# Optimization experiments

Hardware: AMD Instinct MI355X
Metric: run time of the kernel (lower is better)

## Reference

```python
import jax, jax.numpy as jnp
import numpy as np

B, N, C = 8, 4096, 640
H_HEADS = 5
HD = C // H_HEADS  # 128
KS = 5
FOCUS = 3.0
EPS = 1e-6


def setup_inputs() -> dict:
    key = jax.random.key(0)
    ks = jax.random.split(key, 12)
    s = 0.02
    return {
        "x1": jax.random.normal(ks[0], (B, N, C), jnp.float32),
        "x2": jax.random.normal(ks[1], (B, N, C), jnp.float32),
        "Wq": jax.random.normal(ks[2], (C, C), jnp.float32) * s,
        "Wkv": jax.random.normal(ks[3], (2 * C, C), jnp.float32) * s,
        "Wproj": jax.random.normal(ks[4], (C, C), jnp.float32) * s,
        "bproj": jax.random.normal(ks[5], (C,), jnp.float32) * s,
        "dwc_w": jax.random.normal(ks[6], (HD, 1, KS, KS), jnp.float32) * s,
        "dwc_b": jax.random.normal(ks[7], (HD,), jnp.float32) * s,
        "scale": jax.random.normal(ks[8], (1, 1, C), jnp.float32) * s,
        "pos_enc": jax.random.normal(ks[9], (1, N, C), jnp.float32) * s,
        "H": 64,
        "W": 64,
    }


def _split_heads(t):
    # [B, N, C] -> [(B*h), N, hd]
    b, n, c = t.shape
    return t.reshape(b, n, H_HEADS, HD).transpose(0, 2, 1, 3).reshape(b * H_HEADS, n, HD)


def reference(x1, x2, Wq, Wkv, Wproj, bproj, dwc_w, dwc_b, scale, pos_enc, H, W):
    b, n, c = x1.shape
    # note the module's naming swap: self.q projects x2 into v
    v = x2 @ Wq.T                               # [B,N,C]
    kv = (x1 @ Wkv.T).reshape(b, n, 2, c)       # sr_ratio == 1 path
    k = kv[:, :, 0, :] + pos_enc
    q = kv[:, :, 1, :]

    sc = jax.nn.softplus(scale)                 # [1,1,C]
    q = (jax.nn.relu(q) + EPS) / sc
    k = (jax.nn.relu(k) + EPS) / sc
    q_norm = jnp.linalg.norm(q, axis=-1, keepdims=True)
    k_norm = jnp.linalg.norm(k, axis=-1, keepdims=True)
    q = q ** FOCUS
    k = k ** FOCUS
    q = q / jnp.linalg.norm(q, axis=-1, keepdims=True) * q_norm
    k = k / jnp.linalg.norm(k, axis=-1, keepdims=True) * k_norm

    q, k, v = _split_heads(q), _split_heads(k), _split_heads(v)  # [(B*h), N, hd]
    i, j, cc, d = q.shape[-2], k.shape[-2], k.shape[-1], v.shape[-1]
    z = 1.0 / (jnp.einsum('bic,bc->bi', q, k.sum(axis=1)) + EPS)  # [(B*h), N]
    if i * j * (cc + d) > cc * d * (i + j):
        kv2 = jnp.einsum('bjc,bjd->bcd', k, v)                    # [(B*h), hd, hd]
        x = jnp.einsum('bic,bcd,bi->bid', q, kv2, z)
    else:
        qk = jnp.einsum('bic,bjc->bij', q, k)
        x = jnp.einsum('bij,bjd,bi->bid', qk, v, z)

    # depthwise conv feature map on v: 'b (w h) c -> b c w h'
    num = int(round(n ** 0.5))
    fm = v.reshape(v.shape[0], num, num, HD).transpose(0, 3, 1, 2)  # [(B*h), hd, num, num]
    fm = jax.lax.conv_general_dilated(
        fm, dwc_w, window_strides=(1, 1), padding=((KS // 2, KS // 2),) * 2,
        dimension_numbers=('NCHW', 'OIHW', 'NCHW'), feature_group_count=HD)
    fm = fm + dwc_b[None, :, None, None]
    fm = fm.transpose(0, 2, 3, 1).reshape(v.shape[0], n, HD)

    x = x + fm
    # '(b h) n c -> b n (h c)'
    x = x.reshape(b, H_HEADS, n, HD).transpose(0, 2, 1, 3).reshape(b, n, c)
    return x @ Wproj.T + bproj
```

## Files before the change

kernel.cpp:

```cpp
#include <hip/hip_runtime.h>
#include <math.h>

constexpr int CB  = 8;
constexpr int CN  = 4096;
constexpr int CC  = 640;
constexpr int CNH = 5;
constexpr int CHD = 128;
constexpr int CM  = CB * CN;
constexpr float CEPS = 1e-6f;
constexpr int NCH = 8;

typedef __attribute__((ext_vector_type(8))) short bf16x8;
typedef __attribute__((ext_vector_type(4))) float f32x4;

typedef __attribute__((address_space(1))) const unsigned int gas_u32;
typedef __attribute__((address_space(3))) unsigned int las_u32;

__device__ __forceinline__ void gload16(const void* g, void* l) {
    __builtin_amdgcn_global_load_lds((gas_u32*)g, (las_u32*)l, 16, 0, 0);
}

__device__ __forceinline__ short f2bf(float x) {
    unsigned u = __float_as_uint(x);
    unsigned r = (u + 0x7fffu + ((u >> 16) & 1u)) >> 16;
    return (short)r;
}
__device__ __forceinline__ float b2f(unsigned short u) {
    return __uint_as_float(((unsigned)u) << 16);
}

__global__ void softplus_k(const float* __restrict__ scale, float* __restrict__ sc) {
    int t = threadIdx.x;
    if (t < CC) sc[t] = log1pf(expf(scale[t]));
}

__global__ __launch_bounds__(256) void cvt_bf16(const float* __restrict__ src,
                                                unsigned short* __restrict__ dst, int n8) {
    int i = blockIdx.x * 256 + threadIdx.x;
    const int stride = gridDim.x * 256;
    for (; i < n8; i += stride) {
        float4 f0 = *(const float4*)(src + (size_t)i * 8);
        float4 f1 = *(const float4*)(src + (size_t)i * 8 + 4);
        bf16x8 h;
        h[0]=f2bf(f0.x); h[1]=f2bf(f0.y); h[2]=f2bf(f0.z); h[3]=f2bf(f0.w);
        h[4]=f2bf(f1.x); h[5]=f2bf(f1.y); h[6]=f2bf(f1.z); h[7]=f2bf(f1.w);
        *(bf16x8*)(dst + (size_t)i * 8) = h;
    }
}

template<bool BIAS, bool OUTBF>
__global__ __launch_bounds__(256) void gemm_bf16b(const unsigned short* __restrict__ Abf,
                                                  const unsigned short* __restrict__ Bbf,
                                                  void* __restrict__ Co,
                                                  const float* __restrict__ bias,
                                                  int Kr, int Nr) {
    __shared__ unsigned short lA[4096];
    __shared__ unsigned short lB[4096];
    const int t  = threadIdx.x;
    const int m0 = blockIdx.y * 128;
    const int n0 = blockIdx.x * 128;
    const int l  = t & 63, w = t >> 6, wr = w >> 1, wc = w & 1;

    const int cp0 = w * 64 + l;
    const int cp1 = cp0 + 256;
    const int s0 = cp0 ^ (((cp0 >> 2) & 7) ^ ((cp0 >> 4) & 1));
    const int s1 = cp1 ^ (((cp1 >> 2) & 7) ^ ((cp1 >> 4) & 1));
    const size_t gA0 = (size_t)(m0 + (s0 >> 2)) * Kr + (s0 & 3) * 8;
    const size_t gA1 = (size_t)(m0 + (s1 >> 2)) * Kr + (s1 & 3) * 8;
    const size_t gB0 = (size_t)(n0 + (s0 >> 2)) * Kr + (s0 & 3) * 8;
    const size_t gB1 = (size_t)(n0 + (s1 >> 2)) * Kr + (s1 & 3) * 8;
    unsigned short* lA0 = lA + w * 512;
    unsigned short* lA1 = lA + 2048 + w * 512;
    unsigned short* lB0 = lB + w * 512;
    unsigned short* lB1 = lB + 2048 + w * 512;

    const int offA = ((wr * 64 + (l & 15)) * 64 + (l >> 4) * 16) ^ ((l & 7) << 4);
    const int offB = ((wc * 64 + (l & 15)) * 64 + (l >> 4) * 16) ^ ((l & 7) << 4);

    f32x4 acc[4][4];
    #pragma unroll
    for (int i = 0; i < 4; ++i)
        #pragma unroll
        for (int j = 0; j < 4; ++j) acc[i][j] = (f32x4){0.f, 0.f, 0.f, 0.f};

    for (int k0 = 0; k0 < Kr; k0 += 32) {
        gload16(Abf + gA0 + k0, lA0);
        gload16(Abf + gA1 + k0, lA1);
        gload16(Bbf + gB0 + k0, lB0);
        gload16(Bbf + gB1 + k0, lB1);
        __syncthreads();
        bf16x8 af[4], bfv[4];
        #pragma unroll
        for (int i = 0; i < 4; ++i) {
            af[i]  = *(const bf16x8*)((const char*)lA + offA + i * 1024);
            bfv[i] = *(const bf16x8*)((const char*)lB + offB + i * 1024);
        }
        #pragma unroll
        for (int i = 0; i < 4; ++i)
            #pragma unroll
            for (int j = 0; j < 4; ++j)
                acc[i][j] = __builtin_amdgcn_mfma_f32_16x16x32_bf16(af[i], bfv[j], acc[i][j], 0, 0, 0);
        __syncthreads();
    }

    #pragma unroll
    for (int j = 0; j < 4; ++j) {
        const int n = n0 + wc * 64 + j * 16 + (l & 15);
        const float bv = BIAS ? bias[n] : 0.f;
        #pragma unroll
        for (int i = 0; i < 4; ++i) {
            const int m = m0 + wr * 64 + i * 16 + (l >> 4) * 4;
            #pragma unroll
            for (int r = 0; r < 4; ++r) {
                float val = acc[i][j][r] + bv;
                if (OUTBF) ((unsigned short*)Co)[(size_t)(m + r) * Nr + n] = (unsigned short)f2bf(val);
                else       ((float*)Co)[(size_t)(m + r) * Nr + n] = val;
            }
        }
    }
}

__global__ __launch_bounds__(256) void rowtrans2(const unsigned short* __restrict__ qg,
                                                 const unsigned short* __restrict__ kg,
                                                 const float* __restrict__ pos,
                                                 const float* __restrict__ sc,
                                                 unsigned short* __restrict__ qt,
                                                 unsigned short* __restrict__ kt) {
    const int m = blockIdx.x;
    const int n = m & (CN - 1);
    const int t = threadIdx.x;
    float qv[3], kv[3];
    float s2q = 0.f, s6q = 0.f, s2k = 0.f, s6k = 0.f;
    #pragma unroll
    for (int i = 0; i < 3; ++i) {
        int c = t + i * 256;
        if (c < CC) {
            float scv = sc[c];
            float qq = b2f(qg[(size_t)m * CC + c]);
            qq = (fmaxf(qq, 0.f) + CEPS) / scv;
            float kk = b2f(kg[(size_t)m * CC + c]) + pos[(size_t)n * CC + c];
            kk = (fmaxf(kk, 0.f) + CEPS) / scv;
            qv[i] = qq; kv[i] = kk;
            float q2 = qq * qq, k2 = kk * kk;
            s2q += q2; s6q += q2 * q2 * q2;
            s2k += k2; s6k += k2 * k2 * k2;
        } else { qv[i] = 0.f; kv[i] = 0.f; }
    }
    #pragma unroll
    for (int o = 32; o > 0; o >>= 1) {
        s2q += __shfl_down(s2q, o);
        s6q += __shfl_down(s6q, o);
        s2k += __shfl_down(s2k, o);
        s6k += __shfl_down(s6k, o);
    }
    __shared__ float red[4][4];
    const int lane = t & 63, w = t >> 6;
    if (lane == 0) { red[0][w] = s2q; red[1][w] = s6q; red[2][w] = s2k; red[3][w] = s6k; }
    __syncthreads();
    float t2q = red[0][0] + red[0][1] + red[0][2] + red[0][3];
    float t6q = red[1][0] + red[1][1] + red[1][2] + red[1][3];
    float t2k = red[2][0] + red[2][1] + red[2][2] + red[2][3];
    float t6k = red[3][0] + red[3][1] + red[3][2] + red[3][3];
    const float qmul = sqrtf(t2q) / sqrtf(t6q);
    const float kmul = sqrtf(t2k) / sqrtf(t6k);
    #pragma unroll
    for (int i = 0; i < 3; ++i) {
        int c = t + i * 256;
        if (c < CC) {
            qt[(size_t)m * CC + c] = (unsigned short)f2bf(qv[i] * qv[i] * qv[i] * qmul);
            kt[(size_t)m * CC + c] = (unsigned short)f2bf(kv[i] * kv[i] * kv[i] * kmul);
        }
    }
}

__global__ __launch_bounds__(256) void kv2_partial(const unsigned short* __restrict__ kt,
                                                   const unsigned short* __restrict__ vb,
                                                   float* __restrict__ kv2p,
                                                   float* __restrict__ ksmp) {
    const int nc = blockIdx.x, bh = blockIdx.y;
    const int b = bh / CNH, h = bh % CNH;
    __shared__ float ks[32][132];
    __shared__ float vs[32][132];
    const int t = threadIdx.x;
    const int tx = t & 15, ty = t >> 4;
    float acc[8][8];
    #pragma unroll
    for (int i = 0; i < 8; ++i)
        #pragma unroll
        for (int j = 0; j < 8; ++j) acc[i][j] = 0.f;
    float ksacc = 0.f;
    const size_t mbase = (size_t)b * CN + (size_t)nc * 512;
    for (int tile = 0; tile < 16; ++tile) {
        const int nt0 = tile * 32;
        __syncthreads();
        #pragma unroll
        for (int r = 0; r < 2; ++r) {
            int idx = t + 256 * r;
            int nn = idx >> 4, c8 = (idx & 15) * 8;
            size_t g = (mbase + nt0 + nn) * CC + h * CHD + c8;
            bf16x8 hk = *(const bf16x8*)(kt + g);
            bf16x8 hv = *(const bf16x8*)(vb + g);
            float4 k0, k1, v0, v1;
            k0.x=b2f(hk[0]); k0.y=b2f(hk[1]); k0.z=b2f(hk[2]); k0.w=b2f(hk[3]);
            k1.x=b2f(hk[4]); k1.y=b2f(hk[5]); k1.z=b2f(hk[6]); k1.w=b2f(hk[7]);
            v0.x=b2f(hv[0]); v0.y=b2f(hv[1]); v0.z=b2f(hv[2]); v0.w=b2f(hv[3]);
            v1.x=b2f(hv[4]); v1.y=b2f(hv[5]); v1.z=b2f(hv[6]); v1.w=b2f(hv[7]);
            *(float4*)&ks[nn][c8]     = k0;
            *(float4*)&ks[nn][c8 + 4] = k1;
            *(float4*)&vs[nn][c8]     = v0;
            *(float4*)&vs[nn][c8 + 4] = v1;
        }
        __syncthreads();
        #pragma unroll 2
        for (int nn = 0; nn < 32; ++nn) {
            float4 a0 = *(const float4*)&ks[nn][ty*8];
            float4 a1 = *(const float4*)&ks[nn][ty*8+4];
            float4 b0 = *(const float4*)&vs[nn][tx*8];
            float4 b1 = *(const float4*)&vs[nn][tx*8+4];
            float a[8] = {a0.x,a0.y,a0.z,a0.w,a1.x,a1.y,a1.z,a1.w};
            float b[8] = {b0.x,b0.y,b0.z,b0.w,b1.x,b1.y,b1.z,b1.w};
            #pragma unroll
            for (int i = 0; i < 8; ++i)
                #pragma unroll
                for (int j = 0; j < 8; ++j)
                    acc[i][j] = fmaf(a[i], b[j], acc[i][j]);
        }
        if (t < 128) {
            #pragma unroll
            for (int nn = 0; nn < 32; ++nn) ksacc += ks[nn][t];
        }
    }
    float* outp = kv2p + ((size_t)bh * NCH + nc) * 16384;
    #pragma unroll
    for (int i = 0; i < 8; ++i) {
        float4 o0, o1;
        o0.x=acc[i][0]; o0.y=acc[i][1]; o0.z=acc[i][2]; o0.w=acc[i][3];
        o1.x=acc[i][4]; o1.y=acc[i][5]; o1.z=acc[i][6]; o1.w=acc[i][7];
        *(float4*)&outp[(ty*8+i)*128 + tx*8]     = o0;
        *(float4*)&outp[(ty*8+i)*128 + tx*8 + 4] = o1;
    }
    if (t < 128) ksmp[((size_t)bh * NCH + nc) * 128 + t] = ksacc;
}

__global__ __launch_bounds__(256) void kv2_reduce(const float* __restrict__ kv2p,
                                                  const float* __restrict__ ksmp,
                                                  unsigned short* __restrict__ kv2bf,
                                                  float* __restrict__ ksm) {
    const int bh = blockIdx.x, t = threadIdx.x;
    for (int o = t; o < 16384; o += 256) {
        const int d = o >> 7, c = o & 127;
        float s = 0.f;
        #pragma unroll
        for (int nc = 0; nc < NCH; ++nc)
            s += kv2p[((size_t)bh * NCH + nc) * 16384 + c * 128 + d];
        kv2bf[(size_t)bh * 16384 + o] = (unsigned short)f2bf(s);
    }
    if (t < 128) {
        float s = 0.f;
        #pragma unroll
        for (int nc = 0; nc < NCH; ++nc) s += ksmp[((size_t)bh * NCH + nc) * 128 + t];
        ksm[(size_t)bh * 128 + t] = s;
    }
}

__global__ __launch_bounds__(256) void attn_mfma(const unsigned short* __restrict__ qt,
                                                 const unsigned short* __restrict__ kv2bf,
                                                 const float* __restrict__ ksm,
                                                 unsigned short* __restrict__ attb) {
    const int nb = blockIdx.x, bh = blockIdx.y;
    const int b = bh / CNH, h = bh % CNH;
    __shared__ short lQ[16384];
    __shared__ short lKV[16384];
    __shared__ float zs[128];
    const int t = threadIdx.x;
    const int l = t & 63, w = t >> 6, wr = w >> 1, wc = w & 1;
    const size_t m0 = (size_t)b * CN + (size_t)nb * 128;

    const int srow0 = t >> 4;
    const int c16   = t & 15;
    float kreg[8];
    {
        const float* kp = ksm + (size_t)bh * 128 + c16 * 8;
        float4 k0 = *(const float4*)kp, k1 = *(const float4*)(kp + 4);
        kreg[0]=k0.x; kreg[1]=k0.y; kreg[2]=k0.z; kreg[3]=k0.w;
        kreg[4]=k1.x; kreg[5]=k1.y; kreg[6]=k1.z; kreg[7]=k1.w;
    }
    #pragma unroll
    for (int p = 0; p < 8; ++p) {
        const int row = srow0 + p * 16;
        const int st = (row * 256 + c16 * 16) ^ ((row & 7) << 4);
        bf16x8 hq = *(const bf16x8*)(qt + (m0 + row) * CC + h * CHD + c16 * 8);
        *(bf16x8*)((char*)lQ + st) = hq;
        float zp = 0.f;
        #pragma unroll
        for (int j = 0; j < 8; ++j) zp = fmaf(b2f((unsigned short)hq[j]), kreg[j], zp);
        zp += __shfl_xor(zp, 1);
        zp += __shfl_xor(zp, 2);
        zp += __shfl_xor(zp, 4);
        zp += __shfl_xor(zp, 8);
        if (c16 == 0) zs[row] = 1.f / (zp + CEPS);
        bf16x8 hk = *(const bf16x8*)(kv2bf + (size_t)bh * 16384 + row * 128 + c16 * 8);
        *(bf16x8*)((char*)lKV + st) = hk;
    }
    __syncthreads();

    const int baseA = (wr * 64 + (l & 15)) * 256 + ((l >> 4) << 4);
    const int baseB = (wc * 64 + (l & 15)) * 256 + ((l >> 4) << 4);
    const int xorv  = (l & 7) << 4;
    f32x4 acc[4][4];
    #pragma unroll
    for (int i = 0; i < 4; ++i)
        #pragma unroll
        for (int j = 0; j < 4; ++j) acc[i][j] = (f32x4){0.f, 0.f, 0.f, 0.f};

    #pragma unroll
    for (int kk = 0; kk < 4; ++kk) {
        bf16x8 af[4], bv[4];
        #pragma unroll
        for (int i = 0; i < 4; ++i) {
            af[i] = *(const bf16x8*)((const char*)lQ  + (((baseA + kk * 64) ^ xorv) + i * 4096));
            bv[i] = *(const bf16x8*)((const char*)lKV + (((baseB + kk * 64) ^ xorv) + i * 4096));
        }
        #pragma unroll
        for (int i = 0; i < 4; ++i)
            #pragma unroll
            for (int j = 0; j < 4; ++j)
                acc[i][j] = __builtin_amdgcn_mfma_f32_16x16x32_bf16(af[i], bv[j], acc[i][j], 0, 0, 0);
    }

    #pragma unroll
    for (int i = 0; i < 4; ++i) {
        const int mBase = wr * 64 + i * 16 + (l >> 4) * 4;
        float zv[4];
        #pragma unroll
        for (int r = 0; r < 4; ++r) zv[r] = zs[mBase + r];
        #pragma unroll
        for (int j = 0; j < 4; ++j) {
            const int n = wc * 64 + j * 16 + (l & 15);
            unsigned short* op = attb + (m0 + mBase) * CC + h * CHD + n;
            #pragma unroll
            for (int r = 0; r < 4; ++r)
                op[(size_t)r * CC] = (unsigned short)f2bf(acc[i][j][r] * zv[r]);
        }
    }
}

__global__ __launch_bounds__(256) void dwconv2(const unsigned short* __restrict__ vb,
                                               const unsigned short* __restrict__ attb,
                                               const float* __restrict__ w,
                                               const float* __restrict__ bias,
                                               unsigned short* __restrict__ xb) {
    const int yt = blockIdx.x;
    const int dq = blockIdx.y;
    const int bh = blockIdx.z;
    const int b = bh / CNH, h = bh % CNH;
    __shared__ unsigned short vt[12 * 68 * 32];
    const int t = threadIdx.x;
    const int y0 = yt * 8;
    const size_t rowbase = (size_t)b * CN;
    const int cbase = h * CHD + dq * 32;
    for (int c = t; c < 3264; c += 256) {
        int pos = c >> 2, d8 = (c & 3) * 8;
        int ly = pos / 68, lx = pos - ly * 68;
        int yy = y0 - 2 + ly, xx = lx - 2;
        bf16x8 val = (bf16x8){0,0,0,0,0,0,0,0};
        if (yy >= 0 && yy < 64 && xx >= 0 && xx < 64)
            val = *(const bf16x8*)(vb + (rowbase + yy * 64 + xx) * CC + cbase + d8);
        *(bf16x8*)(vt + pos * 32 + d8) = val;
    }
    __syncthreads();
    const int dp = t & 15;
    const int xg = t >> 4;
    const int d0 = dq * 32 + dp * 2;
    float wr0[25], wr1[25];
    #pragma unroll
    for (int i = 0; i < 25; ++i) {
        wr0[i] = w[d0 * 25 + i];
        wr1[i] = w[(d0 + 1) * 25 + i];
    }
    const float bv0 = bias[d0], bv1 = bias[d0 + 1];
    const int x0 = xg * 4;
    for (int oy = 0; oy < 8; ++oy) {
        float a0[4] = {bv0, bv0, bv0, bv0}, a1[4] = {bv1, bv1, bv1, bv1};
        #pragma unroll
        for (int dy = 0; dy < 5; ++dy) {
            const unsigned short* rp = vt + ((oy + dy) * 68 + x0) * 32 + dp * 2;
            float v0[8], v1[8];
            #pragma unroll
            for (int j = 0; j < 8; ++j) {
                unsigned pr = *(const unsigned*)(rp + j * 32);
                v0[j] = __uint_as_float(pr << 16);
                v1[j] = __uint_as_float(pr & 0xffff0000u);
            }
            #pragma unroll
            for (int dx = 0; dx < 5; ++dx) {
                const float w0 = wr0[dy * 5 + dx], w1 = wr1[dy * 5 + dx];
                #pragma unroll
                for (int xo = 0; xo < 4; ++xo) {
                    a0[xo] = fmaf(w0, v0[xo + dx], a0[xo]);
                    a1[xo] = fmaf(w1, v1[xo + dx], a1[xo]);
                }
            }
        }
        #pragma unroll
        for (int xo = 0; xo < 4; ++xo) {
            size_t g = (rowbase + (y0 + oy) * 64 + x0 + xo) * CC + cbase + dp * 2;
            unsigned ap = *(const unsigned*)(attb + g);
            float at0 = __uint_as_float(ap << 16);
            float at1 = __uint_as_float(ap & 0xffff0000u);
            unsigned short o0 = (unsigned short)f2bf(a0[xo] + at0);
            unsigned short o1 = (unsigned short)f2bf(a1[xo] + at1);
            *(unsigned*)(xb + g) = (unsigned)o0 | ((unsigned)o1 << 16);
        }
    }
}

extern "C" void kernel_launch(void* const* d_in, const int* in_sizes, int n_in,
                              void* d_out, int out_size, void* d_ws, size_t ws_size,
                              hipStream_t stream) {
    (void)in_sizes; (void)n_in; (void)out_size; (void)ws_size;
    const float* x1    = (const float*)d_in[0];
    const float* x2    = (const float*)d_in[1];
    const float* Wq    = (const float*)d_in[2];
    const float* Wkv   = (const float*)d_in[3];
    const float* Wproj = (const float*)d_in[4];
    const float* bproj = (const float*)d_in[5];
    const float* dwcw  = (const float*)d_in[6];
    const float* dwcb  = (const float*)d_in[7];
    const float* scale = (const float*)d_in[8];
    const float* pos   = (const float*)d_in[9];
    float* out = (float*)d_out;

    const size_t MC = (size_t)CM * CC;
    unsigned short* ws16 = (unsigned short*)d_ws;
    unsigned short* x1bf  = ws16;
    float*          kv2p  = (float*)ws16;
    unsigned short* attbf = ws16;
    unsigned short* x2bf = ws16 + MC;
    unsigned short* qgbf = x2bf;
    unsigned short* xbf  = x2bf;
    unsigned short* vbf  = ws16 + 2 * MC;
    unsigned short* qtbf = ws16 + 3 * MC;
    unsigned short* kv2bf = ws16 + 4 * MC;
    float* ksmp = (float*)(kv2bf + (size_t)40 * 16384);
    float* ksm  = ksmp + (size_t)40 * NCH * 128;
    float* scb  = ksm + (size_t)40 * 128;
    unsigned short* Wqbf    = (unsigned short*)(scb + 640);
    unsigned short* Wkvbf   = Wqbf + (size_t)CC * CC;
    unsigned short* Wprojbf = Wkvbf + (size_t)2 * CC * CC;
    unsigned short* kgbf = (unsigned short*)d_out;
    unsigned short* ktbf = kgbf + MC;

    hipLaunchKernelGGL(softplus_k, dim3(1), dim3(640), 0, stream, scale, scb);
    hipLaunchKernelGGL(cvt_bf16, dim3(2048), dim3(256), 0, stream, x1, x1bf, (int)(MC / 8));
    hipLaunchKernelGGL(cvt_bf16, dim3(2048), dim3(256), 0, stream, x2, x2bf, (int)(MC / 8));
    hipLaunchKernelGGL(cvt_bf16, dim3(64),  dim3(256), 0, stream, Wq,    Wqbf,    CC * CC / 8);
    hipLaunchKernelGGL(cvt_bf16, dim3(128), dim3(256), 0, stream, Wkv,   Wkvbf,   2 * CC * CC / 8);
    hipLaunchKernelGGL(cvt_bf16, dim3(64),  dim3(256), 0, stream, Wproj, Wprojbf, CC * CC / 8);

    hipLaunchKernelGGL((gemm_bf16b<false, true>), dim3(CC/128, CM/128), dim3(256), 0, stream,
                       x2bf, Wqbf, (void*)vbf, (const float*)nullptr, CC, CC);
    hipLaunchKernelGGL((gemm_bf16b<false, true>), dim3(CC/128, CM/128), dim3(256), 0, stream,
                       x1bf, Wkvbf, (void*)kgbf, (const float*)nullptr, CC, CC);
    hipLaunchKernelGGL((gemm_bf16b<false, true>), dim3(CC/128, CM/128), dim3(256), 0, stream,
                       x1bf, Wkvbf + (size_t)CC * CC, (void*)qgbf, (const float*)nullptr, CC, CC);
    hipLaunchKernelGGL(rowtrans2, dim3(CM), dim3(256), 0, stream, qgbf, kgbf, pos, scb, qtbf, ktbf);
    hipLaunchKernelGGL(kv2_partial, dim3(NCH, 40), dim3(256), 0, stream, ktbf, vbf, kv2p, ksmp);
    hipLaunchKernelGGL(kv2_reduce, dim3(40), dim3(256), 0, stream, kv2p, ksmp, kv2bf, ksm);
    hipLaunchKernelGGL(attn_mfma, dim3(CN/128, 40), dim3(256), 0, stream, qtbf, kv2bf, ksm, attbf);
    hipLaunchKernelGGL(dwconv2, dim3(8, 4, 40), dim3(256), 0, stream, vbf, attbf, dwcw, dwcb, xbf);
    hipLaunchKernelGGL((gemm_bf16b<true, false>), dim3(CC/128, CM/128), dim3(256), 0, stream,
                       xbf, Wprojbf, (void*)out, bproj, CC, CC);
}
```

Measured before the change: 595.2 us.

## Double-buffer GEMM LDS, fuse KV projections, warp-per-row rowtrans, split kv2 into quadrants

The bf16 GEMM now double-buffers its LDS tiles, so the loads for the next k-slice are issued before the MFMAs on the current one, with one barrier per iteration. The two Wkv projections become a single GEMM writing interleaved 1280-wide rows. rowtrans2 handles one row per wavefront using only shuffle reductions, with no shared memory or block barrier. kv2_partial splits each 128x128 output into four 64x64 quadrants to raise the block count, and kv2_reduce is updated to match the new layout. In exchange the GEMM uses twice the LDS and kv2 loads K/V tiles redundantly across quadrants.

```diff
diff --git a/kernel.cpp b/kernel.cpp
--- a/kernel.cpp
+++ b/kernel.cpp
@@ -54,8 +54,8 @@
                                                   void* __restrict__ Co,
                                                   const float* __restrict__ bias,
                                                   int Kr, int Nr) {
-    __shared__ unsigned short lA[4096];
-    __shared__ unsigned short lB[4096];
+    __shared__ unsigned short lA[2][4096];
+    __shared__ unsigned short lB[2][4096];
     const int t  = threadIdx.x;
     const int m0 = blockIdx.y * 128;
     const int n0 = blockIdx.x * 128;
@@ -69,10 +69,8 @@
     const size_t gA1 = (size_t)(m0 + (s1 >> 2)) * Kr + (s1 & 3) * 8;
     const size_t gB0 = (size_t)(n0 + (s0 >> 2)) * Kr + (s0 & 3) * 8;
     const size_t gB1 = (size_t)(n0 + (s1 >> 2)) * Kr + (s1 & 3) * 8;
-    unsigned short* lA0 = lA + w * 512;
-    unsigned short* lA1 = lA + 2048 + w * 512;
-    unsigned short* lB0 = lB + w * 512;
-    unsigned short* lB1 = lB + 2048 + w * 512;
+    const int dA0 = w * 512;
+    const int dA1 = 2048 + w * 512;
 
     const int offA = ((wr * 64 + (l & 15)) * 64 + (l >> 4) * 16) ^ ((l & 7) << 4);
     const int offB = ((wc * 64 + (l & 15)) * 64 + (l >> 4) * 16) ^ ((l & 7) << 4);
@@ -83,17 +81,26 @@
         #pragma unroll
         for (int j = 0; j < 4; ++j) acc[i][j] = (f32x4){0.f, 0.f, 0.f, 0.f};
 
+    gload16(Abf + gA0, &lA[0][dA0]);
+    gload16(Abf + gA1, &lA[0][dA1]);
+    gload16(Bbf + gB0, &lB[0][dA0]);
+    gload16(Bbf + gB1, &lB[0][dA1]);
+    __syncthreads();
+
+    int cur = 0;
     for (int k0 = 0; k0 < Kr; k0 += 32) {
-        gload16(Abf + gA0 + k0, lA0);
-        gload16(Abf + gA1 + k0, lA1);
-        gload16(Bbf + gB0 + k0, lB0);
-        gload16(Bbf + gB1 + k0, lB1);
-        __syncthreads();
+        if (k0 + 32 < Kr) {
+            const int nb = cur ^ 1;
+            gload16(Abf + gA0 + k0 + 32, &lA[nb][dA0]);
+            gload16(Abf + gA1 + k0 + 32, &lA[nb][dA1]);
+            gload16(Bbf + gB0 + k0 + 32, &lB[nb][dA0]);
+            gload16(Bbf + gB1 + k0 + 32, &lB[nb][dA1]);
+        }
         bf16x8 af[4], bfv[4];
         #pragma unroll
         for (int i = 0; i < 4; ++i) {
-            af[i]  = *(const bf16x8*)((const char*)lA + offA + i * 1024);
-            bfv[i] = *(const bf16x8*)((const char*)lB + offB + i * 1024);
+            af[i]  = *(const bf16x8*)((const char*)&lA[cur][0] + offA + i * 1024);
+            bfv[i] = *(const bf16x8*)((const char*)&lB[cur][0] + offB + i * 1024);
         }
         #pragma unroll
         for (int i = 0; i < 4; ++i)
@@ -101,6 +108,7 @@
             for (int j = 0; j < 4; ++j)
                 acc[i][j] = __builtin_amdgcn_mfma_f32_16x16x32_bf16(af[i], bfv[j], acc[i][j], 0, 0, 0);
         __syncthreads();
+        cur ^= 1;
     }
 
     #pragma unroll
@@ -120,56 +128,43 @@
     }
 }
 
-__global__ __launch_bounds__(256) void rowtrans2(const unsigned short* __restrict__ qg,
-                                                 const unsigned short* __restrict__ kg,
+__global__ __launch_bounds__(256) void rowtrans2(const unsigned short* __restrict__ kq,
                                                  const float* __restrict__ pos,
                                                  const float* __restrict__ sc,
                                                  unsigned short* __restrict__ qt,
                                                  unsigned short* __restrict__ kt) {
-    const int m = blockIdx.x;
+    const int w = threadIdx.x >> 6, l = threadIdx.x & 63;
+    const int m = blockIdx.x * 4 + w;
     const int n = m & (CN - 1);
-    const int t = threadIdx.x;
-    float qv[3], kv[3];
+    const unsigned short* rowk = kq + (size_t)m * 1280;
+    const unsigned short* rowq = rowk + 640;
+    float qv[10], kv[10];
     float s2q = 0.f, s6q = 0.f, s2k = 0.f, s6k = 0.f;
     #pragma unroll
-    for (int i = 0; i < 3; ++i) {
-        int c = t + i * 256;
-        if (c < CC) {
-            float scv = sc[c];
-            float qq = b2f(qg[(size_t)m * CC + c]);
-            qq = (fmaxf(qq, 0.f) + CEPS) / scv;
-            float kk = b2f(kg[(size_t)m * CC + c]) + pos[(size_t)n * CC + c];
-            kk = (fmaxf(kk, 0.f) + CEPS) / scv;
-            qv[i] = qq; kv[i] = kk;
-            float q2 = qq * qq, k2 = kk * kk;
-            s2q += q2; s6q += q2 * q2 * q2;
-            s2k += k2; s6k += k2 * k2 * k2;
-        } else { qv[i] = 0.f; kv[i] = 0.f; }
+    for (int j = 0; j < 10; ++j) {
+        const int c = l + 64 * j;
+        const float scv = sc[c];
+        float qq = (fmaxf(b2f(rowq[c]), 0.f) + CEPS) / scv;
+        float kk = (fmaxf(b2f(rowk[c]) + pos[(size_t)n * CC + c], 0.f) + CEPS) / scv;
+        qv[j] = qq; kv[j] = kk;
+        const float q2 = qq * qq, k2 = kk * kk;
+        s2q += q2; s6q += q2 * q2 * q2;
+        s2k += k2; s6k += k2 * k2 * k2;
     }
     #pragma unroll
     for (int o = 32; o > 0; o >>= 1) {
-        s2q += __shfl_down(s2q, o);
-        s6q += __shfl_down(s6q, o);
-        s2k += __shfl_down(s2k, o);
-        s6k += __shfl_down(s6k, o);
-    }
-    __shared__ float red[4][4];
-    const int lane = t & 63, w = t >> 6;
-    if (lane == 0) { red[0][w] = s2q; red[1][w] = s6q; red[2][w] = s2k; red[3][w] = s6k; }
-    __syncthreads();
-    float t2q = red[0][0] + red[0][1] + red[0][2] + red[0][3];
-    float t6q = red[1][0] + red[1][1] + red[1][2] + red[1][3];
-    float t2k = red[2][0] + red[2][1] + red[2][2] + red[2][3];
-    float t6k = red[3][0] + red[3][1] + red[3][2] + red[3][3];
-    const float qmul = sqrtf(t2q) / sqrtf(t6q);
-    const float kmul = sqrtf(t2k) / sqrtf(t6k);
-    #pragma unroll
-    for (int i = 0; i < 3; ++i) {
-        int c = t + i * 256;
-        if (c < CC) {
-            qt[(size_t)m * CC + c] = (unsigned short)f2bf(qv[i] * qv[i] * qv[i] * qmul);
-            kt[(size_t)m * CC + c] = (unsigned short)f2bf(kv[i] * kv[i] * kv[i] * kmul);
-        }
+        s2q += __shfl_xor(s2q, o);
+        s6q += __shfl_xor(s6q, o);
+        s2k += __shfl_xor(s2k, o);
+        s6k += __shfl_xor(s6k, o);
+    }
+    const float qmul = sqrtf(s2q) / sqrtf(s6q);
+    const float kmul = sqrtf(s2k) / sqrtf(s6k);
+    #pragma unroll
+    for (int j = 0; j < 10; ++j) {
+        const int c = l + 64 * j;
+        qt[(size_t)m * CC + c] = (unsigned short)f2bf(qv[j] * qv[j] * qv[j] * qmul);
+        kt[(size_t)m * CC + c] = (unsigned short)f2bf(kv[j] * kv[j] * kv[j] * kmul);
     }
 }
 
@@ -177,69 +172,67 @@
                                                    const unsigned short* __restrict__ vb,
                                                    float* __restrict__ kv2p,
                                                    float* __restrict__ ksmp) {
-    const int nc = blockIdx.x, bh = blockIdx.y;
+    const int nc = blockIdx.x, bh = blockIdx.y, q = blockIdx.z;
+    const int qc = q & 1, qd = q >> 1;
     const int b = bh / CNH, h = bh % CNH;
-    __shared__ float ks[32][132];
-    __shared__ float vs[32][132];
+    __shared__ float ks[32][68];
+    __shared__ float vs[32][68];
     const int t = threadIdx.x;
     const int tx = t & 15, ty = t >> 4;
-    float acc[8][8];
-    #pragma unroll
-    for (int i = 0; i < 8; ++i)
-        #pragma unroll
-        for (int j = 0; j < 8; ++j) acc[i][j] = 0.f;
+    float acc[4][4];
+    #pragma unroll
+    for (int i = 0; i < 4; ++i)
+        #pragma unroll
+        for (int j = 0; j < 4; ++j) acc[i][j] = 0.f;
     float ksacc = 0.f;
     const size_t mbase = (size_t)b * CN + (size_t)nc * 512;
+    const int cofK = h * CHD + qc * 64;
+    const int cofV = h * CHD + qd * 64;
+    const int token = t >> 3, c8 = (t & 7) * 8;
     for (int tile = 0; tile < 16; ++tile) {
         const int nt0 = tile * 32;
         __syncthreads();
-        #pragma unroll
-        for (int r = 0; r < 2; ++r) {
-            int idx = t + 256 * r;
-            int nn = idx >> 4, c8 = (idx & 15) * 8;
-            size_t g = (mbase + nt0 + nn) * CC + h * CHD + c8;
-            bf16x8 hk = *(const bf16x8*)(kt + g);
-            bf16x8 hv = *(const bf16x8*)(vb + g);
+        {
+            const size_t r = (mbase + nt0 + token) * CC;
+            bf16x8 hk = *(const bf16x8*)(kt + r + cofK + c8);
+            bf16x8 hv = *(const bf16x8*)(vb + r + cofV + c8);
             float4 k0, k1, v0, v1;
             k0.x=b2f(hk[0]); k0.y=b2f(hk[1]); k0.z=b2f(hk[2]); k0.w=b2f(hk[3]);
             k1.x=b2f(hk[4]); k1.y=b2f(hk[5]); k1.z=b2f(hk[6]); k1.w=b2f(hk[7]);
             v0.x=b2f(hv[0]); v0.y=b2f(hv[1]); v0.z=b2f(hv[2]); v0.w=b2f(hv[3]);
             v1.x=b2f(hv[4]); v1.y=b2f(hv[5]); v1.z=b2f(hv[6]); v1.w=b2f(hv[7]);
-            *(float4*)&ks[nn][c8]     = k0;
-            *(float4*)&ks[nn][c8 + 4] = k1;
-            *(float4*)&vs[nn][c8]     = v0;
-            *(float4*)&vs[nn][c8 + 4] = v1;
+            *(float4*)&ks[token][c8]     = k0;
+            *(float4*)&ks[token][c8 + 4] = k1;
+            *(float4*)&vs[token][c8]     = v0;
+            *(float4*)&vs[token][c8 + 4] = v1;
         }
         __syncthreads();
-        #pragma unroll 2
+        #pragma unroll 4
         for (int nn = 0; nn < 32; ++nn) {
-            float4 a0 = *(const float4*)&ks[nn][ty*8];
-            float4 a1 = *(const float4*)&ks[nn][ty*8+4];
-            float4 b0 = *(const float4*)&vs[nn][tx*8];
-            float4 b1 = *(const float4*)&vs[nn][tx*8+4];
-            float a[8] = {a0.x,a0.y,a0.z,a0.w,a1.x,a1.y,a1.z,a1.w};
-            float b[8] = {b0.x,b0.y,b0.z,b0.w,b1.x,b1.y,b1.z,b1.w};
-            #pragma unroll
-            for (int i = 0; i < 8; ++i)
+            float4 av = *(const float4*)&ks[nn][ty * 4];
+            float4 bv = *(const float4*)&vs[nn][tx * 4];
+            float a[4] = {av.x, av.y, av.z, av.w};
+            float bb[4] = {bv.x, bv.y, bv.z, bv.w};
+            #pragma unroll
+            for (int i = 0; i < 4; ++i)
                 #pragma unroll
-                for (int j = 0; j < 8; ++j)
-                    acc[i][j] = fmaf(a[i], b[j], acc[i][j]);
-        }
-        if (t < 128) {
+                for (int j = 0; j < 4; ++j)
+                    acc[i][j] = fmaf(a[i], bb[j], acc[i][j]);
+        }
+        if (qd == 0 && t < 64) {
             #pragma unroll
             for (int nn = 0; nn < 32; ++nn) ksacc += ks[nn][t];
         }
     }
-    float* outp = kv2p + ((size_t)bh * NCH + nc) * 16384;
-    #pragma unroll
-    for (int i = 0; i < 8; ++i) {
-        float4 o0, o1;
-        o0.x=acc[i][0]; o0.y=acc[i][1]; o0.z=acc[i][2]; o0.w=acc[i][3];
-        o1.x=acc[i][4]; o1.y=acc[i][5]; o1.z=acc[i][6]; o1.w=acc[i][7];
-        *(float4*)&outp[(ty*8+i)*128 + tx*8]     = o0;
-        *(float4*)&outp[(ty*8+i)*128 + tx*8 + 4] = o1;
-    }
-    if (t < 128) ksmp[((size_t)bh * NCH + nc) * 128 + t] = ksacc;
+    float* outp = kv2p + (((size_t)bh * NCH + nc) * 4 + q) * 4096;
+    #pragma unroll
+    for (int i = 0; i < 4; ++i) {
+        float4 o;
+        o.x = acc[i][0]; o.y = acc[i][1]; o.z = acc[i][2]; o.w = acc[i][3];
+        *(float4*)&outp[(ty * 4 + i) * 64 + tx * 4] = o;
+    }
+    if (qd == 0 && t < 64)
+        ksmp[(((size_t)bh * NCH + nc) * 2 + qc) * 64 + t] = ksacc;
 }
 
 __global__ __launch_bounds__(256) void kv2_reduce(const float* __restrict__ kv2p,
@@ -249,16 +242,18 @@
     const int bh = blockIdx.x, t = threadIdx.x;
     for (int o = t; o < 16384; o += 256) {
         const int d = o >> 7, c = o & 127;
+        const int q = (d >> 6) * 2 + (c >> 6);
         float s = 0.f;
         #pragma unroll
         for (int nc = 0; nc < NCH; ++nc)
-            s += kv2p[((size_t)bh * NCH + nc) * 16384 + c * 128 + d];
+            s += kv2p[(((size_t)bh * NCH + nc) * 4 + q) * 4096 + (c & 63) * 64 + (d & 63)];
         kv2bf[(size_t)bh * 16384 + o] = (unsigned short)f2bf(s);
     }
     if (t < 128) {
         float s = 0.f;
         #pragma unroll
-        for (int nc = 0; nc < NCH; ++nc) s += ksmp[((size_t)bh * NCH + nc) * 128 + t];
+        for (int nc = 0; nc < NCH; ++nc)
+            s += ksmp[(((size_t)bh * NCH + nc) * 2 + (t >> 6)) * 64 + (t & 63)];
         ksm[(size_t)bh * 128 + t] = s;
     }
 }
@@ -437,7 +432,7 @@
     float*          kv2p  = (float*)ws16;
     unsigned short* attbf = ws16;
     unsigned short* x2bf = ws16 + MC;
-    unsigned short* qgbf = x2bf;
+    unsigned short* ktbf = x2bf;
     unsigned short* xbf  = x2bf;
     unsigned short* vbf  = ws16 + 2 * MC;
     unsigned short* qtbf = ws16 + 3 * MC;
@@ -448,8 +443,7 @@
     unsigned short* Wqbf    = (unsigned short*)(scb + 640);
     unsigned short* Wkvbf   = Wqbf + (size_t)CC * CC;
     unsigned short* Wprojbf = Wkvbf + (size_t)2 * CC * CC;
-    unsigned short* kgbf = (unsigned short*)d_out;
-    unsigned short* ktbf = kgbf + MC;
+    unsigned short* kqbf = (unsigned short*)d_out;
 
     hipLaunchKernelGGL(softplus_k, dim3(1), dim3(640), 0, stream, scale, scb);
     hipLaunchKernelGGL(cvt_bf16, dim3(2048), dim3(256), 0, stream, x1, x1bf, (int)(MC / 8));
@@ -460,12 +454,10 @@
 
     hipLaunchKernelGGL((gemm_bf16b<false, true>), dim3(CC/128, CM/128), dim3(256), 0, stream,
                        x2bf, Wqbf, (void*)vbf, (const float*)nullptr, CC, CC);
-    hipLaunchKernelGGL((gemm_bf16b<false, true>), dim3(CC/128, CM/128), dim3(256), 0, stream,
-                       x1bf, Wkvbf, (void*)kgbf, (const float*)nullptr, CC, CC);
-    hipLaunchKernelGGL((gemm_bf16b<false, true>), dim3(CC/128, CM/128), dim3(256), 0, stream,
-                       x1bf, Wkvbf + (size_t)CC * CC, (void*)qgbf, (const float*)nullptr, CC, CC);
-    hipLaunchKernelGGL(rowtrans2, dim3(CM), dim3(256), 0, stream, qgbf, kgbf, pos, scb, qtbf, ktbf);
-    hipLaunchKernelGGL(kv2_partial, dim3(NCH, 40), dim3(256), 0, stream, ktbf, vbf, kv2p, ksmp);
+    hipLaunchKernelGGL((gemm_bf16b<false, true>), dim3(1280/128, CM/128), dim3(256), 0, stream,
+                       x1bf, Wkvbf, (void*)kqbf, (const float*)nullptr, CC, 1280);
+    hipLaunchKernelGGL(rowtrans2, dim3(CM/4), dim3(256), 0, stream, kqbf, pos, scb, qtbf, ktbf);
+    hipLaunchKernelGGL(kv2_partial, dim3(NCH, 40, 4), dim3(256), 0, stream, ktbf, vbf, kv2p, ksmp);
     hipLaunchKernelGGL(kv2_reduce, dim3(40), dim3(256), 0, stream, kv2p, ksmp, kv2bf, ksm);
     hipLaunchKernelGGL(attn_mfma, dim3(CN/128, 40), dim3(256), 0, stream, qtbf, kv2bf, ksm, attbf);
     hipLaunchKernelGGL(dwconv2, dim3(8, 4, 40), dim3(256), 0, stream, vbf, attbf, dwcw, dwcb, xbf);
```

New measurement: 536.2 us. -9.9%, faster.
